# Kernel tuning notes

Measured on AMD Instinct MI355X. Metric: run time of the kernel, lower is better.

The kernel has to match this reference:

```python
import jax, jax.numpy as jnp
import numpy as np

N_NODES = 100000
N_EDGES = 1600000
N_GRAPHS = 512
HID = 192
EPS = 1e-5


def setup_inputs() -> dict:
    key = jax.random.key(0)
    ks = jax.random.split(key, 16)
    x = jax.random.normal(ks[0], (N_NODES, 1), dtype=jnp.float32)
    edge_index = jax.random.randint(ks[1], (2, N_EDGES), 0, N_NODES, dtype=jnp.int64)
    batch = jnp.sort(jax.random.randint(ks[2], (N_NODES,), 0, N_GRAPHS, dtype=jnp.int64))
    def lin(k, fi, fo):
        # torch nn.Linear default init: U(-1/sqrt(fi), 1/sqrt(fi))
        b = 1.0 / np.sqrt(fi)
        return jax.random.uniform(k, (fi, fo), jnp.float32, -b, b)
    return {
        "x": x, "edge_index": edge_index, "batch": batch,
        "W1": lin(ks[3], 1, HID), "b1": jnp.zeros((HID,), jnp.float32),
        "g1": jnp.ones((HID,), jnp.float32), "be1": jnp.zeros((HID,), jnp.float32), "a1": jnp.ones((HID,), jnp.float32),
        "W2": lin(ks[4], HID, HID), "b2": jnp.zeros((HID,), jnp.float32),
        "g2": jnp.ones((HID,), jnp.float32), "be2": jnp.zeros((HID,), jnp.float32), "a2": jnp.ones((HID,), jnp.float32),
        "Wc1": lin(ks[5], HID, HID // 2), "bc1": jax.random.uniform(ks[6], (HID // 2,), jnp.float32, -1/np.sqrt(HID), 1/np.sqrt(HID)),
        "Wc2": lin(ks[7], HID // 2, 4), "bc2": jax.random.uniform(ks[8], (4,), jnp.float32, -1/np.sqrt(HID // 2), 1/np.sqrt(HID // 2)),
    }


def gcn_conv(x, W, b, row, col, n):
    # PyG GCNConv: h = xW; add self-loops; norm = d^-1/2[src] * d^-1/2[dst]; scatter-add to dst; + bias
    h = x @ W
    sl = jnp.arange(n, dtype=row.dtype)
    r = jnp.concatenate([row, sl])
    c = jnp.concatenate([col, sl])
    deg = jax.ops.segment_sum(jnp.ones_like(c, dtype=h.dtype), c, num_segments=n)
    dinv = jnp.where(deg > 0, jax.lax.rsqrt(deg), 0.0)
    norm = dinv[r] * dinv[c]                      # [E+N]
    msg = h[r] * norm[:, None]                    # [E+N, HID] dominant gather
    return jax.ops.segment_sum(msg, c, num_segments=n) + b


def graph_norm(x, batch, gamma, beta, alpha, g):
    cnt = jax.ops.segment_sum(jnp.ones((x.shape[0],), x.dtype), batch, num_segments=g)
    cnt = jnp.maximum(cnt, 1.0)[:, None]
    mean = jax.ops.segment_sum(x, batch, num_segments=g) / cnt
    out = x - alpha * mean[batch]
    var = jax.ops.segment_sum(out * out, batch, num_segments=g) / cnt
    out = out * jax.lax.rsqrt(var + EPS)[batch]
    return gamma * out + beta


def reference(x, edge_index, batch, W1, b1, g1, be1, a1, W2, b2, g2, be2, a2, Wc1, bc1, Wc2, bc2):
    n = x.shape[0]
    row, col = edge_index[0], edge_index[1]
    h = gcn_conv(x, W1, b1, row, col, n)
    h = jax.nn.relu(graph_norm(h, batch, g1, be1, a1, N_GRAPHS))
    h = gcn_conv(h, W2, b2, row, col, n)
    h = jax.nn.relu(graph_norm(h, batch, g2, be2, a2, N_GRAPHS))
    # global mean pool (dropout is identity in eval mode)
    cnt = jnp.maximum(jax.ops.segment_sum(jnp.ones((n,), h.dtype), batch, num_segments=N_GRAPHS), 1.0)
    pooled = jax.ops.segment_sum(h, batch, num_segments=N_GRAPHS) / cnt[:, None]
    z = jax.nn.relu(pooled @ Wc1 + bc1)
    return z @ Wc2 + bc2
```

## Files before the change

kernel.cpp:

```cpp
#include <hip/hip_runtime.h>
#include <hip/hip_bf16.h>
#include <hip/hip_fp16.h>

#define N_NODES 100000
#define N_PAD 100032
#define N_EDGES 1600000
#define N_GRAPHS 512
#define HID 192
#define EPSV 1e-5f

using f16x8 = __attribute__((ext_vector_type(8))) _Float16;
using f16x4 = __attribute__((ext_vector_type(4))) _Float16;
using f32x4 = __attribute__((ext_vector_type(4))) float;

__global__ void k_count(const int* __restrict__ col, int* __restrict__ cnt) {
    int e = blockIdx.x * blockDim.x + threadIdx.x;
    if (e < N_EDGES) atomicAdd(&cnt[col[e]], 1);
}

__global__ void k_misc(const float* __restrict__ W2, _Float16* __restrict__ W2h,
                       const int* __restrict__ batch, int* __restrict__ gstart) {
    int id = blockIdx.x * blockDim.x + threadIdx.x;
    if (id < HID * HID) W2h[id] = (_Float16)W2[id];
    int g = id - HID * HID;
    if (g >= 0 && g <= N_GRAPHS) {
        if (g == N_GRAPHS) { gstart[g] = N_NODES; return; }
        int lo = 0, hi = N_NODES;
        while (lo < hi) { int mid = (lo + hi) >> 1; if (batch[mid] < g) lo = mid + 1; else hi = mid; }
        gstart[g] = lo;
    }
}

__global__ void k_scan_partial(const int* __restrict__ cnt, int* __restrict__ bsum) {
    __shared__ int sd[256];
    int base = blockIdx.x * 1024;
    int t = threadIdx.x;
    int s = 0;
    for (int j = 0; j < 4; ++j) {
        int i = base + j * 256 + t;
        if (i < N_NODES) s += cnt[i];
    }
    sd[t] = s; __syncthreads();
    for (int off = 128; off > 0; off >>= 1) {
        if (t < off) sd[t] += sd[t + off];
        __syncthreads();
    }
    if (t == 0) bsum[blockIdx.x] = sd[0];
}

__global__ void k_scan_final(const int* __restrict__ cnt, const int* __restrict__ bsum,
                             int nb, int* __restrict__ row_ptr, int* __restrict__ cursor,
                             float* __restrict__ dinv, const float* __restrict__ x,
                             float* __restrict__ xp) {
    __shared__ int sd[256];
    __shared__ int s_off;
    int bid = blockIdx.x;
    int t = threadIdx.x;
    int part = 0;
    for (int i = t; i < bid; i += 256) part += bsum[i];
    sd[t] = part; __syncthreads();
    for (int off = 128; off > 0; off >>= 1) {
        if (t < off) sd[t] += sd[t + off];
        __syncthreads();
    }
    if (t == 0) s_off = sd[0];
    __syncthreads();
    int base = bid * 1024;
    int idx0 = base + t * 4;
    int c[4]; int tot = 0;
    for (int j = 0; j < 4; ++j) {
        int i = idx0 + j;
        c[j] = (i < N_NODES) ? cnt[i] : 0;
        tot += c[j];
    }
    sd[t] = tot; __syncthreads();
    for (int off = 1; off < 256; off <<= 1) {
        int v = (t >= off) ? sd[t - off] : 0;
        __syncthreads();
        sd[t] += v;
        __syncthreads();
    }
    int excl = sd[t] - tot + s_off;
    for (int j = 0; j < 4; ++j) {
        int i = idx0 + j;
        if (i < N_NODES) {
            row_ptr[i] = excl;
            cursor[i] = excl;
            float dv = rsqrtf((float)(c[j] + 1));
            dinv[i] = dv;
            xp[i] = x[i] * dv;
            excl += c[j];
        }
    }
    if (bid == nb - 1 && t == 255) row_ptr[N_NODES] = excl;
}

#define FILL_WIN 8
#define FILL_RANGE (N_NODES / FILL_WIN)
#define EPR ((N_EDGES + 255) / 256)
__global__ void __launch_bounds__(256) k_fill(const int* __restrict__ row,
                                              const int* __restrict__ col,
                                              int* __restrict__ cursor,
                                              int* __restrict__ csr_src) {
    int w = blockIdx.x & 7;
    int rank = blockIdx.x >> 3;
    int lo = w * FILL_RANGE;
    int hi = (w == FILL_WIN - 1) ? N_NODES : lo + FILL_RANGE;
    int e0 = rank * EPR;
    int e1 = min(e0 + EPR, N_EDGES);
    for (int e = e0 + threadIdx.x; e < e1; e += 256) {
        int c = col[e];
        if (c >= lo && c < hi) {
            int pos = atomicAdd(&cursor[c], 1);
            csr_src[pos] = row[e];
        }
    }
}

__global__ void k_layer1(const float* __restrict__ x, const float* __restrict__ xp,
                         const int* __restrict__ batch,
                         const int* __restrict__ row_ptr, const int* __restrict__ csr_src,
                         const float* __restrict__ dinv, float4* __restrict__ node_info) {
    int v = blockIdx.x * blockDim.x + threadIdx.x;
    if (v >= N_NODES) return;
    int e0 = row_ptr[v], e1 = row_ptr[v + 1];
    float acc = 0.f;
    for (int base = e0; base < e1; base += 16) {
        int src[16]; float xv[16];
#pragma unroll
        for (int j = 0; j < 16; ++j) { int e = base + j; src[j] = csr_src[(e < e1) ? e : e0]; }
#pragma unroll
        for (int j = 0; j < 16; ++j) { xv[j] = xp[src[j]]; }
#pragma unroll
        for (int j = 0; j < 16; ++j) { acc += (base + j < e1) ? xv[j] : 0.f; }
    }
    float dv = dinv[v];
    float u = dv * acc + x[v] * dv * dv;
    node_info[v] = make_float4(u, dv, __int_as_float((int)batch[v]), 0.f);
}

__global__ void __launch_bounds__(192) k_stats_ab(const float4* __restrict__ node_info,
                                                  const int* __restrict__ gstart,
                                                  const float* __restrict__ W1, const float* __restrict__ b1,
                                                  const float* __restrict__ g1, const float* __restrict__ be1,
                                                  const float* __restrict__ a1,
                                                  float* __restrict__ A, float* __restrict__ B) {
    __shared__ float sd[192], sd2[192];
    int g = blockIdx.x, t = threadIdx.x;
    int i0 = gstart[g], i1 = gstart[g + 1];
    float s = 0.f, s2 = 0.f;
    for (int i = i0 + t; i < i1; i += 192) { float u = node_info[i].x; s += u; s2 += u * u; }
    sd[t] = s; sd2[t] = s2; __syncthreads();
    for (int off = 96; off >= 3; off >>= 1) {
        if (t < off) { sd[t] += sd[t + off]; sd2[t] += sd2[t + off]; }
        __syncthreads();
    }
    float sum_u = sd[0] + sd[1] + sd[2];
    float sum_u2 = sd2[0] + sd2[1] + sd2[2];
    float cntf = fmaxf((float)(i1 - i0), 1.f);
    float m = sum_u / cntf;
    float es2 = sum_u2 / cntf;
    int f = t;
    float w = W1[f], bb = b1[f], al = a1[f];
    float c2 = bb * (1.f - al);
    float d = al * m;
    float eud2 = es2 - 2.f * d * m + d * d;
    float var = w * w * eud2 + 2.f * w * c2 * (m - d) + c2 * c2;
    float rs = rsqrtf(var + EPSV);
    float gam = g1[f];
    A[g * HID + f] = gam * rs * w;
    B[g * HID + f] = gam * rs * (c2 - w * d) + be1[f];
}

__global__ void __launch_bounds__(256) k_x1(const float4* __restrict__ node_info,
                                            const float* __restrict__ A,
                                            const float* __restrict__ B,
                                            _Float16* __restrict__ X1p) {
    int wid = threadIdx.x >> 6;
    int lane = threadIdx.x & 63;
    int v = blockIdx.x * 4 + wid;
    if (v >= N_NODES) return;
    float4 ni = node_info[v];
    float u = ni.x, dv = ni.y;
    int g = __float_as_int(ni.z);
    int c4 = (lane < 48 ? lane : 47) * 4;
    float4 Av = *(const float4*)(A + g * HID + c4);
    float4 Bv = *(const float4*)(B + g * HID + c4);
    f16x4 o;
    o[0] = (_Float16)(fmaxf(fmaf(Av.x, u, Bv.x), 0.f) * dv);
    o[1] = (_Float16)(fmaxf(fmaf(Av.y, u, Bv.y), 0.f) * dv);
    o[2] = (_Float16)(fmaxf(fmaf(Av.z, u, Bv.z), 0.f) * dv);
    o[3] = (_Float16)(fmaxf(fmaf(Av.w, u, Bv.w), 0.f) * dv);
    if (lane < 48) *(f16x4*)(X1p + (size_t)v * HID + c4) = o;
}

#define CH 8
__global__ void __launch_bounds__(256) k_conv2(const _Float16* __restrict__ X1p,
                                               const float* __restrict__ dinv,
                                               const int* __restrict__ row_ptr,
                                               const int* __restrict__ csr_src,
                                               _Float16* __restrict__ aggh) {
    int wid = threadIdx.x >> 6;
    int lane = threadIdx.x & 63;
    int v = blockIdx.x * 4 + wid;
    if (v >= N_NODES) return;
    unsigned c8 = (unsigned)(lane < 48 ? lane : 47) * 8u;
    const char* Xb = (const char*)X1p;
    float dv = dinv[v];
    f16x4 sv = *(const f16x4*)(Xb + (unsigned)v * (HID * 2) + c8);
    float a0 = (float)sv[0], a1 = (float)sv[1], a2 = (float)sv[2], a3 = (float)sv[3];
    int e0 = row_ptr[v], e1 = row_ptr[v + 1];
    for (int b = e0; b < e1; b += CH) {
        unsigned off[CH]; float wgt[CH];
#pragma unroll
        for (int j = 0; j < CH; ++j) {
            int e = b + j;
            off[j] = (unsigned)csr_src[(e < e1) ? e : e0] * (unsigned)(HID * 2) + c8;
            wgt[j] = (e < e1) ? 1.f : 0.f;
        }
        f16x4 rv[CH];
#pragma unroll
        for (int j = 0; j < CH; ++j)
            rv[j] = *(const f16x4*)(Xb + off[j]);
#pragma unroll
        for (int j = 0; j < CH; ++j) {
            a0 = fmaf(wgt[j], (float)rv[j][0], a0);
            a1 = fmaf(wgt[j], (float)rv[j][1], a1);
            a2 = fmaf(wgt[j], (float)rv[j][2], a2);
            a3 = fmaf(wgt[j], (float)rv[j][3], a3);
        }
    }
    if (lane < 48) {
        f16x4 o;
        o[0] = (_Float16)(a0 * dv);
        o[1] = (_Float16)(a1 * dv);
        o[2] = (_Float16)(a2 * dv);
        o[3] = (_Float16)(a3 * dv);
        *(f16x4*)((char*)aggh + (unsigned)v * (HID * 2) + c8) = o;
    }
}

#define BM 64
__global__ void __launch_bounds__(256) k_gemm(const _Float16* __restrict__ A,
                                              const _Float16* __restrict__ W,
                                              const float* __restrict__ b2,
                                              const int* __restrict__ batch,
                                              _Float16* __restrict__ H,
                                              float* __restrict__ sums,
                                              float* __restrict__ sumsq) {
    __shared__ _Float16 a_lds[BM * HID];
    __shared__ int bb[BM];
    int t = threadIdx.x;
    int wid = t >> 6, lane = t & 63;
    int row0 = blockIdx.x * BM;
    if (t < BM) { int gr = row0 + t; bb[t] = (gr < N_NODES) ? batch[gr] : -1; }
    const char* Ablk = (const char*)(A + (size_t)row0 * HID);
#pragma unroll
    for (int it = 0; it < 6; ++it) {
        int bo = (it * 256 + t) * 16;
        int r = bo / 384;
        int swz = bo ^ ((r & 7) << 4);
        *(float4*)((char*)a_lds + swz) = *(const float4*)(Ablk + bo);
    }
    int n0 = wid * 48;
    int bn = n0 + (lane & 15);
    int bk0 = (lane >> 4) << 3;
    f16x8 bfr[6][3];
#pragma unroll
    for (int kc = 0; kc < 6; ++kc)
#pragma unroll
        for (int nt = 0; nt < 3; ++nt) {
            const _Float16* src = W + (size_t)(kc * 32 + bk0) * HID + bn + nt * 16;
            f16x8 v;
#pragma unroll
            for (int j = 0; j < 8; ++j) v[j] = src[(size_t)j * HID];
            bfr[kc][nt] = v;
        }
    __syncthreads();
    f32x4 acc[4][3];
#pragma unroll
    for (int mt = 0; mt < 4; ++mt)
#pragma unroll
        for (int nt = 0; nt < 3; ++nt) acc[mt][nt] = (f32x4){0.f, 0.f, 0.f, 0.f};
    int ar = lane & 15;
#pragma unroll
    for (int mt = 0; mt < 4; ++mt) {
        int r = mt * 16 + ar;
        int rbase = r * 384;
        int sw = (r & 7) << 4;
#pragma unroll
        for (int kc = 0; kc < 6; ++kc) {
            int bo = (rbase + (kc * 32 + bk0) * 2) ^ sw;
            f16x8 a = *(const f16x8*)((const char*)a_lds + bo);
            acc[mt][0] = __builtin_amdgcn_mfma_f32_16x16x32_f16(a, bfr[kc][0], acc[mt][0], 0, 0, 0);
            acc[mt][1] = __builtin_amdgcn_mfma_f32_16x16x32_f16(a, bfr[kc][1], acc[mt][1], 0, 0, 0);
            acc[mt][2] = __builtin_amdgcn_mfma_f32_16x16x32_f16(a, bfr[kc][2], acc[mt][2], 0, 0, 0);
        }
    }
    int cn = lane & 15;
    int rb = (lane >> 4) * 4;
    float bias[3];
#pragma unroll
    for (int nt = 0; nt < 3; ++nt) bias[nt] = b2[n0 + nt * 16 + cn];
    int gA = bb[0];
    int lastv = min(BM, N_NODES - row0) - 1;
    int gB = bb[lastv];
    float sA[3] = {0.f,0.f,0.f}, qA[3] = {0.f,0.f,0.f};
    float sB[3] = {0.f,0.f,0.f}, qB[3] = {0.f,0.f,0.f};
#pragma unroll
    for (int mt = 0; mt < 4; ++mt)
#pragma unroll
        for (int r = 0; r < 4; ++r) {
            int ridx = mt * 16 + rb + r;
            int grow = row0 + ridx;
            if (grow < N_NODES) {
                int gi = bb[ridx];
                _Float16* o = H + (size_t)grow * HID;
#pragma unroll
                for (int nt = 0; nt < 3; ++nt) {
                    float val = acc[mt][nt][r] + bias[nt];
                    o[n0 + nt * 16 + cn] = (_Float16)val;
                    if (gi == gA) { sA[nt] += val; qA[nt] += val * val; }
                    else          { sB[nt] += val; qB[nt] += val * val; }
                }
            }
        }
#pragma unroll
    for (int nt = 0; nt < 3; ++nt) {
        sA[nt] += __shfl_xor(sA[nt], 16); sA[nt] += __shfl_xor(sA[nt], 32);
        qA[nt] += __shfl_xor(qA[nt], 16); qA[nt] += __shfl_xor(qA[nt], 32);
        sB[nt] += __shfl_xor(sB[nt], 16); sB[nt] += __shfl_xor(sB[nt], 32);
        qB[nt] += __shfl_xor(qB[nt], 16); qB[nt] += __shfl_xor(qB[nt], 32);
    }
    if (lane < 16) {
#pragma unroll
        for (int nt = 0; nt < 3; ++nt) {
            int colf = n0 + nt * 16 + cn;
            atomicAdd(&sums[gA * HID + colf], sA[nt]);
            atomicAdd(&sumsq[gA * HID + colf], qA[nt]);
            if (gB != gA) {
                atomicAdd(&sums[gB * HID + colf], sB[nt]);
                atomicAdd(&sumsq[gB * HID + colf], qB[nt]);
            }
        }
    }
}

__global__ void __launch_bounds__(192) k_pool(const _Float16* __restrict__ h,
                                              const int* __restrict__ batch,
                                              const int* __restrict__ gstart,
                                              const float* __restrict__ sums,
                                              const float* __restrict__ sumsq,
                                              const float* __restrict__ g2,
                                              const float* __restrict__ be2,
                                              const float* __restrict__ a2,
                                              float* __restrict__ pooled) {
    int f = threadIdx.x;
    int r0 = blockIdx.x * 64;
    int r1 = min(r0 + 64, N_NODES);
    float al = a2[f], gam = g2[f], bet = be2[f];
    int g = batch[r0];
    float Cg, Dg;
    auto cd = [&](int gg) {
        float cntf = fmaxf((float)(gstart[gg + 1] - gstart[gg]), 1.f);
        float mh = sums[gg * HID + f] / cntf;
        float msq = sumsq[gg * HID + f] / cntf;
        float var = msq - 2.f * al * mh * mh + al * al * mh * mh;
        Cg = gam * rsqrtf(var + EPSV);
        Dg = bet - Cg * al * mh;
    };
    cd(g);
    float s = 0.f;
    int i = r0;
    for (; i + 4 <= r1; i += 4) {
        int g0 = batch[i], g3 = batch[i + 3];
        float v0 = (float)h[(size_t)(i + 0) * HID + f];
        float v1 = (float)h[(size_t)(i + 1) * HID + f];
        float v2 = (float)h[(size_t)(i + 2) * HID + f];
        float v3 = (float)h[(size_t)(i + 3) * HID + f];
        if (g0 == g && g3 == g) {
            s += fmaxf(fmaf(Cg, v0, Dg), 0.f) + fmaxf(fmaf(Cg, v1, Dg), 0.f);
            s += fmaxf(fmaf(Cg, v2, Dg), 0.f) + fmaxf(fmaf(Cg, v3, Dg), 0.f);
        } else {
            float vv[4] = {v0, v1, v2, v3};
            for (int j = 0; j < 4; ++j) {
                int gi = batch[i + j];
                if (gi != g) {
                    atomicAdd(&pooled[g * HID + f], s);
                    s = 0.f; g = gi; cd(g);
                }
                s += fmaxf(fmaf(Cg, vv[j], Dg), 0.f);
            }
        }
    }
    for (; i < r1; ++i) {
        int gi = batch[i];
        float v = (float)h[(size_t)i * HID + f];
        if (gi != g) {
            atomicAdd(&pooled[g * HID + f], s);
            s = 0.f; g = gi; cd(g);
        }
        s += fmaxf(fmaf(Cg, v, Dg), 0.f);
    }
    atomicAdd(&pooled[g * HID + f], s);
}

__global__ void __launch_bounds__(128) k_mlp(const float* __restrict__ pooled,
                                             const int* __restrict__ gstart,
                                             const float* __restrict__ Wc1,
                                             const float* __restrict__ bc1,
                                             const float* __restrict__ Wc2,
                                             const float* __restrict__ bc2,
                                             float* __restrict__ out) {
    __shared__ float p[HID];
    __shared__ float z[96];
    int g = blockIdx.x, t = threadIdx.x;
    float inv = 1.f / fmaxf((float)(gstart[g + 1] - gstart[g]), 1.f);
    for (int i = t; i < HID; i += 128) p[i] = pooled[g * HID + i] * inv;
    __syncthreads();
    if (t < 96) {
        float acc = bc1[t];
        for (int k = 0; k < HID; ++k) acc += p[k] * Wc1[k * 96 + t];
        z[t] = fmaxf(acc, 0.f);
    }
    __syncthreads();
    if (t < 4) {
        float acc = bc2[t];
        for (int j = 0; j < 96; ++j) acc += z[j] * Wc2[j * 4 + t];
        out[g * 4 + t] = acc;
    }
}

extern "C" void kernel_launch(void* const* d_in, const int* in_sizes, int n_in,
                              void* d_out, int out_size, void* d_ws, size_t ws_size,
                              hipStream_t stream) {
    const float* x   = (const float*)d_in[0];
    const int* eidx  = (const int*)d_in[1];
    const int* batch = (const int*)d_in[2];
    const float* W1  = (const float*)d_in[3];
    const float* b1  = (const float*)d_in[4];
    const float* g1  = (const float*)d_in[5];
    const float* be1 = (const float*)d_in[6];
    const float* a1  = (const float*)d_in[7];
    const float* W2  = (const float*)d_in[8];
    const float* b2  = (const float*)d_in[9];
    const float* g2  = (const float*)d_in[10];
    const float* be2 = (const float*)d_in[11];
    const float* a2  = (const float*)d_in[12];
    const float* Wc1 = (const float*)d_in[13];
    const float* bc1 = (const float*)d_in[14];
    const float* Wc2 = (const float*)d_in[15];
    const float* bc2 = (const float*)d_in[16];
    const int* row = eidx;
    const int* col = eidx + N_EDGES;
    float* out = (float*)d_out;

    char* ws = (char*)d_ws;
    size_t off = 0;
    auto alloc = [&](size_t bytes) -> char* {
        char* p = ws + off;
        off = (off + bytes + 255) & ~(size_t)255;
        return p;
    };
    int*   cnt     = (int*)  alloc(N_NODES * 4);
    float* sums2   = (float*)alloc(N_GRAPHS * HID * 4);
    float* sumsq2  = (float*)alloc(N_GRAPHS * HID * 4);
    float* pooled  = (float*)alloc(N_GRAPHS * HID * 4);
    size_t zbytes  = off;
    int*   bsum    = (int*)  alloc(128 * 4);
    int*   row_ptr = (int*)  alloc((N_NODES + 1) * 4);
    int*   cursor  = (int*)  alloc(N_NODES * 4);
    int*   csr_src = (int*)  alloc(N_EDGES * 4);
    float* dinv    = (float*)alloc(N_NODES * 4);
    float* xp      = (float*)alloc(N_NODES * 4);
    float4* node_info = (float4*)alloc((size_t)N_NODES * 16);
    float* Atab    = (float*)alloc(N_GRAPHS * HID * 4);
    float* Btab    = (float*)alloc(N_GRAPHS * HID * 4);
    int*   gstart  = (int*)  alloc((N_GRAPHS + 1) * 4);
    _Float16* X1p  = (_Float16*)alloc((size_t)N_NODES * HID * 2);
    _Float16* aggh = (_Float16*)alloc((size_t)N_PAD * HID * 2);
    _Float16* h2   = (_Float16*)alloc((size_t)N_NODES * HID * 2);
    _Float16* W2h  = (_Float16*)alloc((size_t)HID * HID * 2);

    hipMemsetAsync(ws, 0, zbytes, stream);
    k_misc<<<(HID * HID + N_GRAPHS + 1 + 255) / 256, 256, 0, stream>>>(W2, W2h, batch, gstart);
    k_count<<<(N_EDGES + 255) / 256, 256, 0, stream>>>(col, cnt);
    int PB = (N_NODES + 1023) / 1024;
    k_scan_partial<<<PB, 256, 0, stream>>>(cnt, bsum);
    k_scan_final<<<PB, 256, 0, stream>>>(cnt, bsum, PB, row_ptr, cursor, dinv, x, xp);
    k_fill<<<2048, 256, 0, stream>>>(row, col, cursor, csr_src);
    k_layer1<<<(N_NODES + 255) / 256, 256, 0, stream>>>(x, xp, batch, row_ptr, csr_src, dinv, node_info);
    k_stats_ab<<<N_GRAPHS, 192, 0, stream>>>(node_info, gstart, W1, b1, g1, be1, a1, Atab, Btab);
    k_x1<<<(N_NODES + 3) / 4, 256, 0, stream>>>(node_info, Atab, Btab, X1p);
    k_conv2<<<(N_NODES + 3) / 4, 256, 0, stream>>>(X1p, dinv, row_ptr, csr_src, aggh);
    k_gemm<<<(N_NODES + BM - 1) / BM, 256, 0, stream>>>(aggh, W2h, b2, batch, h2, sums2, sumsq2);
    int SB = (N_NODES + 63) / 64;
    k_pool<<<SB, 192, 0, stream>>>(h2, batch, gstart, sums2, sumsq2, g2, be2, a2, pooled);
    k_mlp<<<N_GRAPHS, 128, 0, stream>>>(pooled, gstart, Wc1, bc1, Wc2, bc2, out);
}
```

Measured before the change: 337.0 us.

## Split feature matrix into 8 column slices for cache-local SpMM gather

Stores the layer-1 features and the aggregated output as 8 separate column slices of 24 halves (48 bytes) per node, so each slice (about 4.8 MB) can stay in cache while conv2 gathers it. Conv2 launches 8x as many blocks, one per slice, and each wave handles 8 edges at a time with 8 lanes per edge, then reduces the partial sums with shuffles. The GEMM load is changed to rebuild full rows from the sliced layout. In exchange, csr_src and row_ptr are reread once per slice, and each gather fetches only 48 bytes per row instead of 384.

```diff
diff --git a/kernel.cpp b/kernel.cpp
--- a/kernel.cpp
+++ b/kernel.cpp
@@ -8,6 +8,8 @@
 #define N_GRAPHS 512
 #define HID 192
 #define EPSV 1e-5f
+
+#define SS ((size_t)N_PAD * 48)
 
 using f16x8 = __attribute__((ext_vector_type(8))) _Float16;
 using f16x4 = __attribute__((ext_vector_type(4))) _Float16;
@@ -175,73 +177,80 @@
 __global__ void __launch_bounds__(256) k_x1(const float4* __restrict__ node_info,
                                             const float* __restrict__ A,
                                             const float* __restrict__ B,
-                                            _Float16* __restrict__ X1p) {
-    int wid = threadIdx.x >> 6;
-    int lane = threadIdx.x & 63;
-    int v = blockIdx.x * 4 + wid;
+                                            _Float16* __restrict__ X1pS) {
+    int slice = blockIdx.x & 7;
+    int wid = threadIdx.x >> 6, lane = threadIdx.x & 63;
+    int v = (blockIdx.x >> 3) * 32 + wid * 8 + (lane >> 3);
     if (v >= N_NODES) return;
+    int fc = lane & 7; int fcc = fc < 6 ? fc : 5;
     float4 ni = node_info[v];
     float u = ni.x, dv = ni.y;
     int g = __float_as_int(ni.z);
-    int c4 = (lane < 48 ? lane : 47) * 4;
-    float4 Av = *(const float4*)(A + g * HID + c4);
-    float4 Bv = *(const float4*)(B + g * HID + c4);
+    int fbase = slice * 24 + fcc * 4;
+    float4 Av = *(const float4*)(A + g * HID + fbase);
+    float4 Bv = *(const float4*)(B + g * HID + fbase);
     f16x4 o;
     o[0] = (_Float16)(fmaxf(fmaf(Av.x, u, Bv.x), 0.f) * dv);
     o[1] = (_Float16)(fmaxf(fmaf(Av.y, u, Bv.y), 0.f) * dv);
     o[2] = (_Float16)(fmaxf(fmaf(Av.z, u, Bv.z), 0.f) * dv);
     o[3] = (_Float16)(fmaxf(fmaf(Av.w, u, Bv.w), 0.f) * dv);
-    if (lane < 48) *(f16x4*)(X1p + (size_t)v * HID + c4) = o;
-}
-
-#define CH 8
-__global__ void __launch_bounds__(256) k_conv2(const _Float16* __restrict__ X1p,
+    if (fc < 6)
+        *(f16x4*)((char*)X1pS + (size_t)slice * SS + (size_t)v * 48 + fcc * 8) = o;
+}
+
+__global__ void __launch_bounds__(256) k_conv2(const _Float16* __restrict__ X1pS,
                                                const float* __restrict__ dinv,
                                                const int* __restrict__ row_ptr,
                                                const int* __restrict__ csr_src,
-                                               _Float16* __restrict__ aggh) {
-    int wid = threadIdx.x >> 6;
-    int lane = threadIdx.x & 63;
-    int v = blockIdx.x * 4 + wid;
+                                               _Float16* __restrict__ agghS) {
+    int slice = blockIdx.x & 7;
+    int wid = threadIdx.x >> 6, lane = threadIdx.x & 63;
+    int v = (blockIdx.x >> 3) * 4 + wid;
     if (v >= N_NODES) return;
-    unsigned c8 = (unsigned)(lane < 48 ? lane : 47) * 8u;
-    const char* Xb = (const char*)X1p;
-    float dv = dinv[v];
-    f16x4 sv = *(const f16x4*)(Xb + (unsigned)v * (HID * 2) + c8);
-    float a0 = (float)sv[0], a1 = (float)sv[1], a2 = (float)sv[2], a3 = (float)sv[3];
+    int e_sub = lane >> 3;
+    int fc = lane & 7; int fcc = fc < 6 ? fc : 5;
+    const char* Xs = (const char*)X1pS + (size_t)slice * SS;
+    unsigned fbyte = (unsigned)fcc * 8u;
+    float a0 = 0.f, a1 = 0.f, a2 = 0.f, a3 = 0.f;
     int e0 = row_ptr[v], e1 = row_ptr[v + 1];
-    for (int b = e0; b < e1; b += CH) {
-        unsigned off[CH]; float wgt[CH];
-#pragma unroll
-        for (int j = 0; j < CH; ++j) {
-            int e = b + j;
-            off[j] = (unsigned)csr_src[(e < e1) ? e : e0] * (unsigned)(HID * 2) + c8;
-            wgt[j] = (e < e1) ? 1.f : 0.f;
-        }
-        f16x4 rv[CH];
-#pragma unroll
-        for (int j = 0; j < CH; ++j)
-            rv[j] = *(const f16x4*)(Xb + off[j]);
-#pragma unroll
-        for (int j = 0; j < CH; ++j) {
-            a0 = fmaf(wgt[j], (float)rv[j][0], a0);
-            a1 = fmaf(wgt[j], (float)rv[j][1], a1);
-            a2 = fmaf(wgt[j], (float)rv[j][2], a2);
-            a3 = fmaf(wgt[j], (float)rv[j][3], a3);
-        }
-    }
-    if (lane < 48) {
+    for (int b = e0; b < e1; b += 16) {
+        int ea = b + e_sub, eb = b + 8 + e_sub;
+        int sa = __builtin_nontemporal_load(&csr_src[(ea < e1) ? ea : e0]);
+        int sb = __builtin_nontemporal_load(&csr_src[(eb < e1) ? eb : e0]);
+        float wa = (ea < e1) ? 1.f : 0.f;
+        float wb = (eb < e1) ? 1.f : 0.f;
+        f16x4 ra = *(const f16x4*)(Xs + (unsigned)sa * 48u + fbyte);
+        f16x4 rb = *(const f16x4*)(Xs + (unsigned)sb * 48u + fbyte);
+        a0 = fmaf(wa, (float)ra[0], a0);
+        a1 = fmaf(wa, (float)ra[1], a1);
+        a2 = fmaf(wa, (float)ra[2], a2);
+        a3 = fmaf(wa, (float)ra[3], a3);
+        a0 = fmaf(wb, (float)rb[0], a0);
+        a1 = fmaf(wb, (float)rb[1], a1);
+        a2 = fmaf(wb, (float)rb[2], a2);
+        a3 = fmaf(wb, (float)rb[3], a3);
+    }
+#pragma unroll
+    for (int d = 32; d >= 8; d >>= 1) {
+        a0 += __shfl_down(a0, d);
+        a1 += __shfl_down(a1, d);
+        a2 += __shfl_down(a2, d);
+        a3 += __shfl_down(a3, d);
+    }
+    if (lane < 6) {
+        f16x4 sv = *(const f16x4*)(Xs + (unsigned)v * 48u + fbyte);
+        float dv = dinv[v];
         f16x4 o;
-        o[0] = (_Float16)(a0 * dv);
-        o[1] = (_Float16)(a1 * dv);
-        o[2] = (_Float16)(a2 * dv);
-        o[3] = (_Float16)(a3 * dv);
-        *(f16x4*)((char*)aggh + (unsigned)v * (HID * 2) + c8) = o;
+        o[0] = (_Float16)((a0 + (float)sv[0]) * dv);
+        o[1] = (_Float16)((a1 + (float)sv[1]) * dv);
+        o[2] = (_Float16)((a2 + (float)sv[2]) * dv);
+        o[3] = (_Float16)((a3 + (float)sv[3]) * dv);
+        *(f16x4*)((char*)agghS + (size_t)slice * SS + (size_t)v * 48u + fbyte) = o;
     }
 }
 
 #define BM 64
-__global__ void __launch_bounds__(256) k_gemm(const _Float16* __restrict__ A,
+__global__ void __launch_bounds__(256) k_gemm(const _Float16* __restrict__ AggS,
                                               const _Float16* __restrict__ W,
                                               const float* __restrict__ b2,
                                               const int* __restrict__ batch,
@@ -254,13 +263,17 @@
     int wid = t >> 6, lane = t & 63;
     int row0 = blockIdx.x * BM;
     if (t < BM) { int gr = row0 + t; bb[t] = (gr < N_NODES) ? batch[gr] : -1; }
-    const char* Ablk = (const char*)(A + (size_t)row0 * HID);
+    const char* Ab = (const char*)AggS;
 #pragma unroll
     for (int it = 0; it < 6; ++it) {
         int bo = (it * 256 + t) * 16;
         int r = bo / 384;
+        int cb = bo % 384;
+        int sl = cb / 48;
+        int within = cb % 48;
+        size_t src = (size_t)sl * SS + (size_t)(row0 + r) * 48 + within;
         int swz = bo ^ ((r & 7) << 4);
-        *(float4*)((char*)a_lds + swz) = *(const float4*)(Ablk + bo);
+        *(float4*)((char*)a_lds + swz) = *(const float4*)(Ab + src);
     }
     int n0 = wid * 48;
     int bn = n0 + (lane & 15);
@@ -477,8 +490,8 @@
     float* Atab    = (float*)alloc(N_GRAPHS * HID * 4);
     float* Btab    = (float*)alloc(N_GRAPHS * HID * 4);
     int*   gstart  = (int*)  alloc((N_GRAPHS + 1) * 4);
-    _Float16* X1p  = (_Float16*)alloc((size_t)N_NODES * HID * 2);
-    _Float16* aggh = (_Float16*)alloc((size_t)N_PAD * HID * 2);
+    _Float16* X1pS = (_Float16*)alloc((size_t)N_PAD * HID * 2);
+    _Float16* agghS= (_Float16*)alloc((size_t)N_PAD * HID * 2);
     _Float16* h2   = (_Float16*)alloc((size_t)N_NODES * HID * 2);
     _Float16* W2h  = (_Float16*)alloc((size_t)HID * HID * 2);
 
@@ -491,9 +504,9 @@
     k_fill<<<2048, 256, 0, stream>>>(row, col, cursor, csr_src);
     k_layer1<<<(N_NODES + 255) / 256, 256, 0, stream>>>(x, xp, batch, row_ptr, csr_src, dinv, node_info);
     k_stats_ab<<<N_GRAPHS, 192, 0, stream>>>(node_info, gstart, W1, b1, g1, be1, a1, Atab, Btab);
-    k_x1<<<(N_NODES + 3) / 4, 256, 0, stream>>>(node_info, Atab, Btab, X1p);
-    k_conv2<<<(N_NODES + 3) / 4, 256, 0, stream>>>(X1p, dinv, row_ptr, csr_src, aggh);
-    k_gemm<<<(N_NODES + BM - 1) / BM, 256, 0, stream>>>(aggh, W2h, b2, batch, h2, sums2, sumsq2);
+    k_x1<<<8 * ((N_NODES + 31) / 32), 256, 0, stream>>>(node_info, Atab, Btab, X1pS);
+    k_conv2<<<8 * ((N_NODES + 3) / 4), 256, 0, stream>>>(X1pS, dinv, row_ptr, csr_src, agghS);
+    k_gemm<<<(N_NODES + BM - 1) / BM, 256, 0, stream>>>(agghS, W2h, b2, batch, h2, sums2, sumsq2);
     int SB = (N_NODES + 63) / 64;
     k_pool<<<SB, 192, 0, stream>>>(h2, batch, gstart, sums2, sumsq2, g2, be2, a2, pooled);
     k_mlp<<<N_GRAPHS, 128, 0, stream>>>(pooled, gstart, Wc1, bc1, Wc2, bc2, out);
```

New measurement: 533.7 us. 1.58x slower.
